# Optimization experiments

Measured on AMD Instinct MI355X. Metric: run time of the kernel, lower is better.

The kernel has to match this reference:

```python
import jax, jax.numpy as jnp
import numpy as np

EMBED, HIDDEN, VOCAB, FEAT_DIM = 256, 512, 10000, 1024
B, NREG, CAPLEN = 128, 49, 33


def setup_inputs() -> dict:
    key = jax.random.key(0)
    ks = jax.random.split(key, 20)
    xav = lambda k, shp: jax.random.uniform(k, shp, jnp.float32, -1.0, 1.0) * jnp.sqrt(6.0 / (shp[0] + shp[1]))
    d = {
        "features": jax.random.normal(ks[0], (B, NREG, FEAT_DIM), jnp.float32),
        "captions": jax.random.randint(ks[1], (B, CAPLEN), 0, VOCAB),
        "emb": jax.random.uniform(ks[2], (VOCAB, EMBED), jnp.float32, -0.1, 0.1),
        "W_ft": jax.random.uniform(ks[3], (EMBED, FEAT_DIM), jnp.float32, -0.1, 0.1),
        "b_ft": jnp.zeros((EMBED,), jnp.float32),
        "W_i": xav(ks[4], (2 * EMBED, HIDDEN)), "U_i": xav(ks[5], (HIDDEN, HIDDEN)), "b_i": jnp.zeros((HIDDEN,), jnp.float32),
        "W_f": xav(ks[6], (2 * EMBED, HIDDEN)), "U_f": xav(ks[7], (HIDDEN, HIDDEN)), "b_f": jnp.zeros((HIDDEN,), jnp.float32),
        "W_c": xav(ks[8], (2 * EMBED, HIDDEN)), "U_c": xav(ks[9], (HIDDEN, HIDDEN)), "b_c": jnp.zeros((HIDDEN,), jnp.float32),
        "W_o": xav(ks[10], (2 * EMBED, HIDDEN)), "U_o": xav(ks[11], (HIDDEN, HIDDEN)), "b_o": jnp.zeros((HIDDEN,), jnp.float32),
        "W_fc": jax.random.uniform(ks[12], (VOCAB, HIDDEN), jnp.float32, -0.1, 0.1),
        "b_fc": jnp.zeros((VOCAB,), jnp.float32),
    }
    return d


def reference(features, captions, emb, W_ft, b_ft,
              W_i, U_i, b_i, W_f, U_f, b_f, W_c, U_c, b_c, W_o, U_o, b_o,
              W_fc, b_fc):
    # mean-pool image regions, project to embed space
    feats_emb = features.mean(axis=1) @ W_ft.T + b_ft            # [B, E]
    embeds = emb[captions[:, :-1]]                                # [B, T, E]
    xs = jnp.swapaxes(embeds, 0, 1)                               # [T, B, E]

    h0 = jnp.zeros((features.shape[0], HIDDEN), features.dtype)
    c0 = jnp.zeros_like(h0)

    def step(carry, e_t):
        h, c = carry
        x = jnp.concatenate([e_t, feats_emb], axis=1)             # [B, 2E] (dropout=eval identity)
        i = jax.nn.sigmoid(x @ W_i + h @ U_i + b_i)
        f = jax.nn.sigmoid(x @ W_f + h @ U_f + b_f)
        g = jnp.tanh(x @ W_c + h @ U_c + b_c)
        o = jax.nn.sigmoid(x @ W_o + h @ U_o + b_o)
        c_new = f * c + i * g
        h_new = o * jnp.tanh(c_new)
        return (h_new, c_new), h_new

    _, hs = jax.lax.scan(step, (h0, c0), xs)                      # hs: [T, B, H]
    outputs = jnp.einsum('tbh,vh->btv', hs, W_fc) + b_fc          # [B, T, V]
    return outputs
```

## Files before the change

kernel.cpp:

```cpp
#include <hip/hip_runtime.h>
#include <hip/hip_bf16.h>

#define EMBED    256
#define HIDDEN   512
#define VOCAB    10000
#define WFC_PAD  10112
#define NTILES   79
#define FEAT_DIM 1024
#define BATCH    128
#define NREGS    49
#define TSTEPS   32

typedef unsigned short u16;
typedef unsigned long long u64;
using f32x4 = __attribute__((ext_vector_type(4))) float;
using s16x8 = __attribute__((ext_vector_type(8))) short;
using u32x4 = __attribute__((ext_vector_type(4))) unsigned;

__device__ __forceinline__ u16 f2bf(float f) {
  __hip_bfloat16 h = __float2bfloat16(f);
  return *reinterpret_cast<u16*>(&h);
}
__device__ __forceinline__ float sig_(float x) {
  return 1.0f / (1.0f + __expf(-x));
}
__device__ __forceinline__ float tanh_(float x) {
  x = fminf(fmaxf(x, -15.f), 15.f);
  float e = __expf(2.f * x);
  return (e - 1.f) / (e + 1.f);
}
__device__ __forceinline__ void gl_lds16(const u16* g, u16* l) {
  __builtin_amdgcn_global_load_lds(
      (const __attribute__((address_space(1))) unsigned*)g,
      (__attribute__((address_space(3))) unsigned*)l, 16, 0, 0);
}

struct GatePtrs {
  const float* W[4];
  const float* U[4];
  const float* b[4];
};

__global__ __launch_bounds__(256)
void k_prep_all(GatePtrs p, const float* __restrict__ features,
                const float* __restrict__ W_ft, const float* __restrict__ b_ft,
                const float* __restrict__ W_fc, float* __restrict__ feats_emb,
                u16* __restrict__ WcatT, u16* __restrict__ UcatT,
                float* __restrict__ bcat, u16* __restrict__ Wfc_bf) {
  __shared__ float sh[64 * 65];
  int bid = blockIdx.x, tid = threadIdx.x;

  if (bid < 128) {
    float* mean = sh;
    int b = bid;
    const float* fb = features + (size_t)b * NREGS * FEAT_DIM;
    for (int d = tid; d < FEAT_DIM; d += 256) {
      float s = 0.f;
      for (int r = 0; r < NREGS; ++r) s += fb[r * FEAT_DIM + d];
      mean[d] = s * (1.0f / 49.0f);
    }
    __syncthreads();
    const float* w = W_ft + (size_t)tid * FEAT_DIM;
    float acc = b_ft[tid];
#pragma unroll 4
    for (int d = 0; d < FEAT_DIM; d += 4) {
      float4 m4 = *(const float4*)&mean[d];
      float4 w4 = *(const float4*)&w[d];
      acc += m4.x * w4.x + m4.y * w4.y + m4.z * w4.z + m4.w * w4.w;
    }
    feats_emb[b * EMBED + tid] = acc;
  } else if (bid < 640) {
    int idx = bid - 128;
    int z = idx >> 8;
    int rem = idx & 255;
    int g = rem >> 6;
    int x = rem & 63;
    float (*tile)[65] = (float(*)[65])sh;
    const float* src = z ? p.U[g] : p.W[g];
    u16* dst = z ? UcatT : WcatT;
    int tj = (x & 7) * 64;
    int tk = (x >> 3) * 64;
    int tx = tid & 63, ty = tid >> 6;
#pragma unroll
    for (int i = 0; i < 16; ++i)
      tile[ty + 4 * i][tx] = src[(size_t)(tk + ty + 4 * i) * HIDDEN + tj + tx];
    __syncthreads();
#pragma unroll
    for (int i = 0; i < 16; ++i)
      dst[(size_t)(g * 512 + tj + ty + 4 * i) * 512 + tk + tx] = f2bf(tile[tx][ty + 4 * i]);
  } else {
    int idx = (bid - 640) * 256 + tid;
    if (idx < WFC_PAD * HIDDEN / 4) {
      size_t e0 = (size_t)idx * 4;
      ushort4 o;
      if (e0 < (size_t)VOCAB * HIDDEN) {
        float4 v = *(const float4*)(W_fc + e0);
        o.x = f2bf(v.x); o.y = f2bf(v.y); o.z = f2bf(v.z); o.w = f2bf(v.w);
      } else {
        o.x = o.y = o.z = o.w = 0;
      }
      *(ushort4*)(Wfc_bf + e0) = o;
    }
    if (idx < 4 * HIDDEN) bcat[idx] = p.b[idx >> 9][idx & 511];
  }
}

__global__ __launch_bounds__(256)
void k_build_x(const float* __restrict__ emb, const int* __restrict__ captions,
               const float* __restrict__ feats_emb, u16* __restrict__ X) {
  int idx = blockIdx.x * 256 + threadIdx.x;
  int r = idx >> 9, col = idx & 511;
  int t = r >> 7, b = r & 127;
  float v;
  if (col < EMBED) {
    int tok = captions[b * 33 + t];
    v = emb[(size_t)tok * EMBED + col];
  } else {
    v = feats_emb[b * EMBED + (col - EMBED)];
  }
  X[idx] = f2bf(v);
}

__global__ __launch_bounds__(256)
void k_gemm_bt(const u16* __restrict__ A, const u16* __restrict__ Bt,
               const float* __restrict__ bias, float* __restrict__ C,
               int M, int N, int K) {
  __shared__ u16 Al[128 * 32];
  __shared__ u16 Bl[128 * 32];
  int tid = threadIdx.x;
  int lane = tid & 63;
  int w = tid >> 6;
  int wr = w & 1, wc = w >> 1;

  int Mtiles = gridDim.y, Ntiles = gridDim.x;
  int nwg = Mtiles * Ntiles;
  int id = blockIdx.y * Ntiles + blockIdx.x;
  int q = nwg >> 3, r = nwg & 7;
  int xcd = id & 7, pos = id >> 3;
  int wg = (xcd < r ? xcd * (q + 1) : r * (q + 1) + (xcd - r) * q) + pos;
  int m0 = (wg % Mtiles) * 128;
  int n0 = (wg / Mtiles) * 128;

  f32x4 acc[4][4];
#pragma unroll
  for (int i = 0; i < 4; ++i)
#pragma unroll
    for (int j = 0; j < 4; ++j) acc[i][j] = (f32x4){0.f, 0.f, 0.f, 0.f};

  int srowq = lane >> 2;
  int skq   = (lane & 3) * 8;

  for (int k0 = 0; k0 < K; k0 += 32) {
    __syncthreads();
#pragma unroll
    for (int i = 0; i < 2; ++i) {
      int rr = w * 32 + i * 16;
      gl_lds16(A + (size_t)(m0 + rr + srowq) * K + k0 + skq, Al + rr * 32);
      gl_lds16(Bt + (size_t)(n0 + rr + srowq) * K + k0 + skq, Bl + rr * 32);
    }
    __syncthreads();

    const u16* ab = Al + (wr * 64 + (lane & 15)) * 32 + (lane >> 4) * 8;
    const u16* bb = Bl + (wc * 64 + (lane & 15)) * 32 + (lane >> 4) * 8;
    s16x8 af[4], bf_[4];
#pragma unroll
    for (int mi = 0; mi < 4; ++mi) af[mi] = *(const s16x8*)(ab + mi * 16 * 32);
#pragma unroll
    for (int ni = 0; ni < 4; ++ni) bf_[ni] = *(const s16x8*)(bb + ni * 16 * 32);
#pragma unroll
    for (int mi = 0; mi < 4; ++mi)
#pragma unroll
      for (int ni = 0; ni < 4; ++ni)
        acc[mi][ni] = __builtin_amdgcn_mfma_f32_16x16x32_bf16(af[mi], bf_[ni], acc[mi][ni], 0, 0, 0);
  }

  int rbase = (lane >> 4) * 4;
  int colf = lane & 15;
#pragma unroll
  for (int mi = 0; mi < 4; ++mi) {
    int mbase = m0 + wr * 64 + mi * 16 + rbase;
#pragma unroll
    for (int ni = 0; ni < 4; ++ni) {
      int n = n0 + wc * 64 + ni * 16 + colf;
      if (n < N) {
        float bv = bias[n];
#pragma unroll
        for (int reg = 0; reg < 4; ++reg)
          C[(size_t)(mbase + reg) * N + n] = acc[mi][ni][reg] + bv;
      }
    }
  }
}

#define USTR 520

__global__ __launch_bounds__(256, 1)
void k_fused(const u16* __restrict__ UcatT, const float* __restrict__ gates_pre,
             unsigned* __restrict__ hx, int* __restrict__ flags, int* __restrict__ ticket,
             const u16* __restrict__ Wfc, const float* __restrict__ b_fc,
             float* __restrict__ out) {
  __shared__ u16 SH[128 * USTR];
  __shared__ int tickLds;
  int tid = threadIdx.x;
  int lane = tid & 63;
  int w = tid >> 6;

  if (blockIdx.x < 64) {
    u16* Ul = SH;
    int wr = w & 1, wj = w >> 1;
    int mg = blockIdx.x >> 4;
    int jb = blockIdx.x & 15;
    int b0 = mg * 32;
    int j0 = jb * 32;

    for (int i = tid; i < 128 * 64; i += 256) {
      int row = i >> 6;
      int kc = (i & 63) * 8;
      int gr = ((row >> 5) << 9) + j0 + (row & 31);
      uint4 v = *(const uint4*)(UcatT + (size_t)gr * 512 + kc);
      *(uint4*)(Ul + row * USTR + kc) = v;
    }
    __syncthreads();

    int jloc = wj * 16 + (lane & 15);
    int jj = j0 + jloc;
    int rb = wr * 16 + (lane >> 4) * 4;
    int arow = b0 + wr * 16 + (lane & 15);
    const u16* ubase = Ul + (size_t)jloc * USTR + (lane >> 4) * 8;
    int* myflag = flags + mg * 16 + jb;
    const int* pollp = flags + mg * 16 + (lane & 15);

    float c[4] = {0.f, 0.f, 0.f, 0.f};
    float gpv[16];

#pragma unroll
    for (int reg = 0; reg < 4; ++reg)
#pragma unroll
      for (int gi = 0; gi < 4; ++gi)
        gpv[reg * 4 + gi] = gates_pre[((size_t)(b0 + rb + reg)) * 2048 + gi * 512 + jj];

#pragma unroll 1
    for (int t = 0; t < TSTEPS; ++t) {
      f32x4 acc[4];
#pragma unroll
      for (int gi = 0; gi < 4; ++gi) acc[gi] = (f32x4){0.f, 0.f, 0.f, 0.f};

      if (t > 0) {
        int fv;
        do {
          asm volatile(
              "global_load_dword %0, %1, off sc0 sc1\n\t"
              "s_waitcnt vmcnt(0)"
              : "=v"(fv) : "v"(pollp) : "memory");
        } while (!__all(fv >= t));

        const u16* hp = (const u16*)hx + ((size_t)(t - 1) * 128 + arow) * 512 + (lane >> 4) * 8;
        u32x4 f[16];
        asm volatile(
            "global_load_dwordx4 %0, %4, off sc0 sc1\n\t"
            "global_load_dwordx4 %1, %4, off offset:64 sc0 sc1\n\t"
            "global_load_dwordx4 %2, %4, off offset:128 sc0 sc1\n\t"
            "global_load_dwordx4 %3, %4, off offset:192 sc0 sc1"
            : "=&v"(f[0]), "=&v"(f[1]), "=&v"(f[2]), "=&v"(f[3])
            : "v"(hp) : "memory");
        asm volatile(
            "global_load_dwordx4 %0, %4, off offset:256 sc0 sc1\n\t"
            "global_load_dwordx4 %1, %4, off offset:320 sc0 sc1\n\t"
            "global_load_dwordx4 %2, %4, off offset:384 sc0 sc1\n\t"
            "global_load_dwordx4 %3, %4, off offset:448 sc0 sc1"
            : "=&v"(f[4]), "=&v"(f[5]), "=&v"(f[6]), "=&v"(f[7])
            : "v"(hp) : "memory");
        asm volatile(
            "global_load_dwordx4 %0, %4, off offset:512 sc0 sc1\n\t"
            "global_load_dwordx4 %1, %4, off offset:576 sc0 sc1\n\t"
            "global_load_dwordx4 %2, %4, off offset:640 sc0 sc1\n\t"
            "global_load_dwordx4 %3, %4, off offset:704 sc0 sc1"
            : "=&v"(f[8]), "=&v"(f[9]), "=&v"(f[10]), "=&v"(f[11])
            : "v"(hp) : "memory");
        asm volatile(
            "global_load_dwordx4 %0, %4, off offset:768 sc0 sc1\n\t"
            "global_load_dwordx4 %1, %4, off offset:832 sc0 sc1\n\t"
            "global_load_dwordx4 %2, %4, off offset:896 sc0 sc1\n\t"
            "global_load_dwordx4 %3, %4, off offset:960 sc0 sc1\n\t"
            "s_waitcnt vmcnt(0)"
            : "=&v"(f[12]), "=&v"(f[13]), "=&v"(f[14]), "=&v"(f[15])
            : "v"(hp) : "memory");
        __builtin_amdgcn_sched_barrier(0);

#pragma unroll
        for (int kk = 0; kk < 16; ++kk) {
          s16x8 af = __builtin_bit_cast(s16x8, f[kk]);
#pragma unroll
          for (int gi = 0; gi < 4; ++gi) {
            s16x8 bf_ = *(const s16x8*)(ubase + (size_t)gi * 32 * USTR + kk * 32);
            acc[gi] = __builtin_amdgcn_mfma_f32_16x16x32_bf16(af, bf_, acc[gi], 0, 0, 0);
          }
        }
      }

#pragma unroll
      for (int reg = 0; reg < 4; ++reg) {
        float pi = acc[0][reg] + gpv[reg * 4 + 0];
        float pf = acc[1][reg] + gpv[reg * 4 + 1];
        float pg = acc[2][reg] + gpv[reg * 4 + 2];
        float po = acc[3][reg] + gpv[reg * 4 + 3];
        float iv = sig_(pi), fv2 = sig_(pf), gv = tanh_(pg), ov = sig_(po);
        float cn = fv2 * c[reg] + iv * gv;
        c[reg] = cn;
        float hn = ov * tanh_(cn);
        u16 hb = f2bf(hn);
        unsigned pv = hb;
        unsigned nv = __shfl_down(pv, 1);
        if ((lane & 1) == 0) {
          unsigned packed = pv | (nv << 16);
          unsigned* dst = hx + ((size_t)t * 128 + b0 + rb + reg) * 256 + (jj >> 1);
          asm volatile("global_store_dword %0, %1, off sc0 sc1"
                       :: "v"(dst), "v"(packed) : "memory");
        }
      }

      __syncthreads();
      if (tid == 0) {
        int fl = t + 1;
        asm volatile("global_store_dword %0, %1, off sc0 sc1"
                     :: "v"(myflag), "v"(fl) : "memory");
      }

      if (t < TSTEPS - 1) {
#pragma unroll
        for (int reg = 0; reg < 4; ++reg)
#pragma unroll
          for (int gi = 0; gi < 4; ++gi)
            gpv[reg * 4 + gi] =
                gates_pre[((size_t)(t + 1) * 128 + b0 + rb + reg) * 2048 + gi * 512 + jj];
      }
    }
  } else {
    u16* Al = SH;
    u16* Bl = SH + 128 * 32;
    int wr = w & 1, wc = w >> 1;
    int srowq = lane >> 2;
    int skq   = (lane & 3) * 8;
    const u16* hx16 = (const u16*)hx;

    for (;;) {
      if (tid == 0)
        tickLds = __hip_atomic_fetch_add(ticket, 1, __ATOMIC_RELAXED, __HIP_MEMORY_SCOPE_AGENT);
      __syncthreads();
      int T = tickLds;
      if (T >= TSTEPS * NTILES) break;
      int t = T / NTILES, nt = T % NTILES;

      if (w == 0) {
        const int* fp = flags + lane;
        for (;;) {
          int fv;
          asm volatile(
              "global_load_dword %0, %1, off sc0 sc1\n\t"
              "s_waitcnt vmcnt(0)"
              : "=v"(fv) : "v"(fp) : "memory");
          if (__all(fv >= t + 1)) break;
          __builtin_amdgcn_s_sleep(64);
        }
      }
      __syncthreads();

      const u16* A = hx16 + (size_t)t * 128 * 512;
      int n0 = nt * 128;

      f32x4 acc[4][4];
#pragma unroll
      for (int i = 0; i < 4; ++i)
#pragma unroll
        for (int j = 0; j < 4; ++j) acc[i][j] = (f32x4){0.f, 0.f, 0.f, 0.f};

      for (int k0 = 0; k0 < HIDDEN; k0 += 32) {
        __syncthreads();
#pragma unroll
        for (int i = 0; i < 2; ++i) {
          int rr = w * 32 + i * 16;
          gl_lds16(A + (size_t)(rr + srowq) * HIDDEN + k0 + skq, Al + rr * 32);
          gl_lds16(Wfc + (size_t)(n0 + rr + srowq) * HIDDEN + k0 + skq, Bl + rr * 32);
        }
        __syncthreads();

        const u16* ab = Al + (wr * 64 + (lane & 15)) * 32 + (lane >> 4) * 8;
        const u16* bb = Bl + (wc * 64 + (lane & 15)) * 32 + (lane >> 4) * 8;
        s16x8 af[4], bf_[4];
#pragma unroll
        for (int mi = 0; mi < 4; ++mi) af[mi] = *(const s16x8*)(ab + mi * 16 * 32);
#pragma unroll
        for (int ni = 0; ni < 4; ++ni) bf_[ni] = *(const s16x8*)(bb + ni * 16 * 32);
#pragma unroll
        for (int mi = 0; mi < 4; ++mi)
#pragma unroll
          for (int ni = 0; ni < 4; ++ni)
            acc[mi][ni] = __builtin_amdgcn_mfma_f32_16x16x32_bf16(af[mi], bf_[ni], acc[mi][ni], 0, 0, 0);
      }

      int rbase = (lane >> 4) * 4;
      int colf = lane & 15;
#pragma unroll
      for (int mi = 0; mi < 4; ++mi) {
        int mbase = wr * 64 + mi * 16 + rbase;
#pragma unroll
        for (int ni = 0; ni < 4; ++ni) {
          int n = n0 + wc * 64 + ni * 16 + colf;
          if (n < VOCAB) {
            float bv = b_fc[n];
#pragma unroll
            for (int reg = 0; reg < 4; ++reg)
              out[(size_t)(mbase + reg) * (TSTEPS * VOCAB) + (size_t)t * VOCAB + n] =
                  acc[mi][ni][reg] + bv;
          }
        }
      }
    }
  }
}

extern "C" void kernel_launch(void* const* d_in, const int* in_sizes, int n_in,
                              void* d_out, int out_size, void* d_ws, size_t ws_size,
                              hipStream_t stream) {
  const float* features = (const float*)d_in[0];
  const int*   captions = (const int*)d_in[1];
  const float* emb      = (const float*)d_in[2];
  const float* W_ft     = (const float*)d_in[3];
  const float* b_ft     = (const float*)d_in[4];
  GatePtrs p;
  p.W[0] = (const float*)d_in[5];  p.U[0] = (const float*)d_in[6];  p.b[0] = (const float*)d_in[7];
  p.W[1] = (const float*)d_in[8];  p.U[1] = (const float*)d_in[9];  p.b[1] = (const float*)d_in[10];
  p.W[2] = (const float*)d_in[11]; p.U[2] = (const float*)d_in[12]; p.b[2] = (const float*)d_in[13];
  p.W[3] = (const float*)d_in[14]; p.U[3] = (const float*)d_in[15]; p.b[3] = (const float*)d_in[16];
  const float* W_fc = (const float*)d_in[17];
  const float* b_fc = (const float*)d_in[18];
  float* out = (float*)d_out;

  char* ws = (char*)d_ws;
  float*    feats_emb = (float*)(ws + 0);
  u16*      X         = (u16*)(ws + 131072);
  u16*      WcatT     = (u16*)(ws + 4325376);
  u16*      UcatT     = (u16*)(ws + 6422528);
  float*    bcat      = (float*)(ws + 8519680);
  u16*      Wfc_bf    = (u16*)(ws + 8527872);
  float*    gates_pre = (float*)(ws + 18882560);
  int*      flags     = (int*)(ws + 52436992);
  int*      ticket    = flags + 64;
  unsigned* hx        = (unsigned*)(ws + 52846592);

  hipMemsetAsync(flags, 0, 512, stream);

  k_prep_all<<<640 + (WFC_PAD * HIDDEN / 4 + 255) / 256, 256, 0, stream>>>(
      p, features, W_ft, b_ft, W_fc, feats_emb, WcatT, UcatT, bcat, Wfc_bf);

  k_build_x<<<(TSTEPS * BATCH * 2 * EMBED) / 256, 256, 0, stream>>>(emb, captions, feats_emb, X);

  k_gemm_bt<<<dim3(2048 / 128, 4096 / 128), 256, 0, stream>>>(
      X, WcatT, bcat, gates_pre, 4096, 2048, 512);

  k_fused<<<256, 256, 0, stream>>>(UcatT, gates_pre, hx, flags, ticket,
                                   Wfc_bf, b_fc, out);
}
```

Measured before the change: 310.1 us.

## Split input-gate GEMM into per-batch feature term and time-varying embedding term

The feature half of the LSTM input is constant across time, so its gate contribution is computed once per batch row in a small GEMM (128x2048, K=256) with the bias folded in. The main gate GEMM now uses only the embedding half (K=256 instead of 512) and adds the precomputed feature term as a per-row bias. The separate build-X kernel is folded into the prep kernel, which gathers the embeddings to bf16 directly. This halves the big GEMM's work and drops one launch, at the cost of an extra small GEMM launch and a gathered bias read in the epilogue.

```diff
diff --git a/kernel.cpp b/kernel.cpp
--- a/kernel.cpp
+++ b/kernel.cpp
@@ -44,9 +44,11 @@
 __global__ __launch_bounds__(256)
 void k_prep_all(GatePtrs p, const float* __restrict__ features,
                 const float* __restrict__ W_ft, const float* __restrict__ b_ft,
-                const float* __restrict__ W_fc, float* __restrict__ feats_emb,
-                u16* __restrict__ WcatT, u16* __restrict__ UcatT,
-                float* __restrict__ bcat, u16* __restrict__ Wfc_bf) {
+                const float* __restrict__ W_fc, const float* __restrict__ emb,
+                const int* __restrict__ captions,
+                u16* __restrict__ feats_bf, u16* __restrict__ WcatT,
+                u16* __restrict__ UcatT, float* __restrict__ bcat,
+                u16* __restrict__ Wfc_bf, u16* __restrict__ X_emb) {
   __shared__ float sh[64 * 65];
   int bid = blockIdx.x, tid = threadIdx.x;
 
@@ -68,7 +70,7 @@
       float4 w4 = *(const float4*)&w[d];
       acc += m4.x * w4.x + m4.y * w4.y + m4.z * w4.z + m4.w * w4.w;
     }
-    feats_emb[b * EMBED + tid] = acc;
+    feats_bf[b * EMBED + tid] = f2bf(acc);
   } else if (bid < 640) {
     int idx = bid - 128;
     int z = idx >> 8;
@@ -88,8 +90,17 @@
 #pragma unroll
     for (int i = 0; i < 16; ++i)
       dst[(size_t)(g * 512 + tj + ty + 4 * i) * 512 + tk + tx] = f2bf(tile[tx][ty + 4 * i]);
+  } else if (bid < 1664) {
+    int idx = (bid - 640) * 256 + tid;
+    int r = idx >> 6, c4 = (idx & 63) * 4;
+    int t = r >> 7, b = r & 127;
+    int tok = captions[b * 33 + t];
+    float4 v = *(const float4*)(emb + (size_t)tok * EMBED + c4);
+    ushort4 o;
+    o.x = f2bf(v.x); o.y = f2bf(v.y); o.z = f2bf(v.z); o.w = f2bf(v.w);
+    *(ushort4*)(X_emb + (size_t)r * EMBED + c4) = o;
   } else {
-    int idx = (bid - 640) * 256 + tid;
+    int idx = (bid - 1664) * 256 + tid;
     if (idx < WFC_PAD * HIDDEN / 4) {
       size_t e0 = (size_t)idx * 4;
       ushort4 o;
@@ -106,25 +117,10 @@
 }
 
 __global__ __launch_bounds__(256)
-void k_build_x(const float* __restrict__ emb, const int* __restrict__ captions,
-               const float* __restrict__ feats_emb, u16* __restrict__ X) {
-  int idx = blockIdx.x * 256 + threadIdx.x;
-  int r = idx >> 9, col = idx & 511;
-  int t = r >> 7, b = r & 127;
-  float v;
-  if (col < EMBED) {
-    int tok = captions[b * 33 + t];
-    v = emb[(size_t)tok * EMBED + col];
-  } else {
-    v = feats_emb[b * EMBED + (col - EMBED)];
-  }
-  X[idx] = f2bf(v);
-}
-
-__global__ __launch_bounds__(256)
-void k_gemm_bt(const u16* __restrict__ A, const u16* __restrict__ Bt,
-               const float* __restrict__ bias, float* __restrict__ C,
-               int M, int N, int K) {
+void k_gemm_bt(const u16* __restrict__ A, int lda,
+               const u16* __restrict__ Bt, int ldb,
+               const float* __restrict__ bias1, const float* __restrict__ bias2,
+               float* __restrict__ C, int M, int N, int K) {
   __shared__ u16 Al[128 * 32];
   __shared__ u16 Bl[128 * 32];
   int tid = threadIdx.x;
@@ -155,8 +151,8 @@
 #pragma unroll
     for (int i = 0; i < 2; ++i) {
       int rr = w * 32 + i * 16;
-      gl_lds16(A + (size_t)(m0 + rr + srowq) * K + k0 + skq, Al + rr * 32);
-      gl_lds16(Bt + (size_t)(n0 + rr + srowq) * K + k0 + skq, Bl + rr * 32);
+      gl_lds16(A + (size_t)(m0 + rr + srowq) * lda + k0 + skq, Al + rr * 32);
+      gl_lds16(Bt + (size_t)(n0 + rr + srowq) * ldb + k0 + skq, Bl + rr * 32);
     }
     __syncthreads();
 
@@ -183,10 +179,12 @@
     for (int ni = 0; ni < 4; ++ni) {
       int n = n0 + wc * 64 + ni * 16 + colf;
       if (n < N) {
-        float bv = bias[n];
-#pragma unroll
-        for (int reg = 0; reg < 4; ++reg)
-          C[(size_t)(mbase + reg) * N + n] = acc[mi][ni][reg] + bv;
+#pragma unroll
+        for (int reg = 0; reg < 4; ++reg) {
+          int mm = mbase + reg;
+          float bv = bias1 ? bias1[n] : bias2[(size_t)(mm & 127) * N + n];
+          C[(size_t)mm * N + n] = acc[mi][ni][reg] + bv;
+        }
       }
     }
   }
@@ -437,8 +435,9 @@
   float* out = (float*)d_out;
 
   char* ws = (char*)d_ws;
-  float*    feats_emb = (float*)(ws + 0);
-  u16*      X         = (u16*)(ws + 131072);
+  u16*      feats_bf  = (u16*)(ws + 0);
+  u16*      X_emb     = (u16*)(ws + 131072);
+  float*    gfeats    = (float*)(ws + 2228224);
   u16*      WcatT     = (u16*)(ws + 4325376);
   u16*      UcatT     = (u16*)(ws + 6422528);
   float*    bcat      = (float*)(ws + 8519680);
@@ -450,13 +449,15 @@
 
   hipMemsetAsync(flags, 0, 512, stream);
 
-  k_prep_all<<<640 + (WFC_PAD * HIDDEN / 4 + 255) / 256, 256, 0, stream>>>(
-      p, features, W_ft, b_ft, W_fc, feats_emb, WcatT, UcatT, bcat, Wfc_bf);
-
-  k_build_x<<<(TSTEPS * BATCH * 2 * EMBED) / 256, 256, 0, stream>>>(emb, captions, feats_emb, X);
-
-  k_gemm_bt<<<dim3(2048 / 128, 4096 / 128), 256, 0, stream>>>(
-      X, WcatT, bcat, gates_pre, 4096, 2048, 512);
+  k_prep_all<<<1664 + (WFC_PAD * HIDDEN / 4 + 255) / 256, 256, 0, stream>>>(
+      p, features, W_ft, b_ft, W_fc, emb, captions,
+      feats_bf, WcatT, UcatT, bcat, Wfc_bf, X_emb);
+
+  k_gemm_bt<<<dim3(16, 1), 256, 0, stream>>>(
+      feats_bf, 256, WcatT + 256, 512, bcat, nullptr, gfeats, 128, 2048, 256);
+
+  k_gemm_bt<<<dim3(16, 32), 256, 0, stream>>>(
+      X_emb, 256, WcatT, 512, nullptr, gfeats, gates_pre, 4096, 2048, 256);
 
   k_fused<<<256, 256, 0, stream>>>(UcatT, gates_pre, hx, flags, ticket,
                                    Wfc_bf, b_fc, out);
```

Result: slower. 323.5 us (+4.3%).
